# Performance work log

Measured on AMD Instinct MI355X. Metric: run time of the kernel, lower is better.

The kernel has to match this reference:

```python
import jax, jax.numpy as jnp
import numpy as np

B, N, DIM, HEADS = 8, 512, 512, 16
MAX_DIST, NG = 128, 32
RBF_STOP = 20.0
EPS = 1e-5


def _ln(x, g, b):
    m = jnp.mean(x, axis=-1, keepdims=True)
    v = jnp.mean((x - m) ** 2, axis=-1, keepdims=True)
    return (x - m) * jax.lax.rsqrt(v + EPS) * g + b


def setup_inputs() -> dict:
    key = jax.random.key(0)
    ks = jax.random.split(key, 12)
    d = DIM
    s = 0.02
    return {
        "x": jax.random.normal(ks[0], (B * N, d), jnp.float32),
        "dist_matrix": jax.random.randint(ks[1], (B, N, N), 0, MAX_DIST, jnp.int32),
        "dist_3d": jax.random.uniform(ks[2], (B, N, N), jnp.float32) * RBF_STOP,
        "norm1_g": jnp.ones((d,), jnp.float32),
        "norm1_b": jnp.zeros((d,), jnp.float32),
        "in_proj_w": jax.random.normal(ks[3], (3 * d, d), jnp.float32) * s,
        "in_proj_b": jnp.zeros((3 * d,), jnp.float32),
        "out_proj_w": jax.random.normal(ks[4], (d, d), jnp.float32) * s,
        "out_proj_b": jnp.zeros((d,), jnp.float32),
        "dist_emb": jax.random.normal(ks[5], (MAX_DIST, HEADS), jnp.float32) * s,
        "rbf_w": jax.random.normal(ks[6], (HEADS, NG), jnp.float32) * s,
        "rbf_b": jnp.zeros((HEADS,), jnp.float32),
        "norm2_g": jnp.ones((d,), jnp.float32),
        "norm2_b": jnp.zeros((d,), jnp.float32),
        "ffn_w1": jax.random.normal(ks[7], (4 * d, d), jnp.float32) * s,
        "ffn_b1": jnp.zeros((4 * d,), jnp.float32),
        "ffn_w2": jax.random.normal(ks[8], (d, 4 * d), jnp.float32) * s,
        "ffn_b2": jnp.zeros((d,), jnp.float32),
        "batch": jnp.repeat(jnp.arange(B, dtype=jnp.int32), N),
    }


def reference(x, dist_matrix, dist_3d, norm1_g, norm1_b, in_proj_w, in_proj_b,
              out_proj_w, out_proj_b, dist_emb, rbf_w, rbf_b, norm2_g, norm2_b,
              ffn_w1, ffn_b1, ffn_w2, ffn_b2, batch):
    b, n = dist_matrix.shape[0], dist_matrix.shape[1]
    d = x.shape[-1]
    dh = d // HEADS
    # equal-size graphs -> to_dense_batch is a reshape, mask all-true
    xd = x.reshape(b, n, d)

    # additive attention bias: shortest-path-distance embedding + RBF projection
    dc = jnp.clip(dist_matrix, 0, MAX_DIST - 1)
    bias_spd = dist_emb[dc]                                  # [b, n, n, H]
    offset = jnp.linspace(0.0, RBF_STOP, NG, dtype=jnp.float32)
    coeff = -0.5 / (RBF_STOP / (NG - 1)) ** 2
    rbf = jnp.exp(coeff * (dist_3d[..., None] - offset) ** 2)  # [b, n, n, NG]
    bias_3d = rbf @ rbf_w.T + rbf_b                          # [b, n, n, H]
    bias = jnp.transpose(bias_spd + bias_3d, (0, 3, 1, 2))   # [b, H, n, n]

    # multi-head attention (pre-norm residual, as in source)
    h = _ln(xd, norm1_g, norm1_b)
    qkv = h @ in_proj_w.T + in_proj_b
    q, k, v = jnp.split(qkv, 3, axis=-1)
    q = q.reshape(b, n, HEADS, dh).transpose(0, 2, 1, 3)
    k = k.reshape(b, n, HEADS, dh).transpose(0, 2, 1, 3)
    v = v.reshape(b, n, HEADS, dh).transpose(0, 2, 1, 3)
    scores = jnp.einsum('bhqd,bhkd->bhqk', q, k) / jnp.sqrt(jnp.float32(dh)) + bias
    attn = jax.nn.softmax(scores, axis=-1)
    ctx = jnp.einsum('bhqk,bhkd->bhqd', attn, v)
    ctx = ctx.transpose(0, 2, 1, 3).reshape(b, n, d)
    attn_out = ctx @ out_proj_w.T + out_proj_b
    h = h + attn_out

    # FFN (dropout inactive at eval)
    h2 = _ln(h, norm2_g, norm2_b)
    ff = jax.nn.gelu(h2 @ ffn_w1.T + ffn_b1, approximate=False) @ ffn_w2.T + ffn_b2
    h = h + ff
    return h.reshape(b * n, d)
```

## Files before the change

kernel.cpp:

```cpp
#include <hip/hip_runtime.h>
#include <hip/hip_bf16.h>
#include <math.h>

#define BB 8
#define NN 512
#define DD 512
#define NH 16
#define DH 32
#define TD 1536
#define NG 32
#define MAXD 128

typedef __attribute__((ext_vector_type(8))) short bf16x8;
typedef __attribute__((ext_vector_type(4))) float f32x4;

__device__ inline short f2bf(float x) {
    __hip_bfloat16 h = __float2bfloat16(x);
    return *reinterpret_cast<short*>(&h);
}
__device__ inline float bf2f(short x) {
    union { unsigned u; float f; } c;
    c.u = ((unsigned)(unsigned short)x) << 16;
    return c.f;
}

__device__ inline void gld_lds16(const void* g, void* l) {
    __builtin_amdgcn_global_load_lds(
        (const __attribute__((address_space(1))) unsigned int*)g,
        (__attribute__((address_space(3))) unsigned int*)l, 16, 0, 0);
}

__global__ __launch_bounds__(256) void cvt_weights(
    const float* __restrict__ s0, const float* __restrict__ s1,
    const float* __restrict__ s2, const float* __restrict__ s3,
    short* __restrict__ d0, short* __restrict__ d1,
    short* __restrict__ d2, short* __restrict__ d3,
    int n0, int n1, int n2, int n3) {
    const float* s; short* d; int n;
    switch (blockIdx.y) {
        case 0: s = s0; d = d0; n = n0; break;
        case 1: s = s1; d = d1; n = n1; break;
        case 2: s = s2; d = d2; n = n2; break;
        default: s = s3; d = d3; n = n3; break;
    }
    const int i = (blockIdx.x * 256 + threadIdx.x) * 4;
    if (i >= n) return;
    const float4 v = *(const float4*)(s + i);
    short4 o;
    o.x = f2bf(v.x); o.y = f2bf(v.y); o.z = f2bf(v.z); o.w = f2bf(v.w);
    *(short4*)(d + i) = o;
}

__global__ __launch_bounds__(256) void rbf_table(
    const float* __restrict__ rbfw, const float* __restrict__ rbfb,
    short* __restrict__ Tg) {
    const int idx = blockIdx.x * 256 + threadIdx.x;
    if (idx >= 130 * 16) return;
    const int i = idx >> 4, h = idx & 15;
    const float STEP  = 20.0f / 31.0f;
    const float COEFF = -0.5f / (STEP * STEP);
    const float x = fminf((float)i, 128.0f) * (20.0f / 128.0f);
    float acc = rbfb[h];
#pragma unroll
    for (int g = 0; g < NG; g++) {
        const float t = x - (float)g * STEP;
        acc += __expf(COEFF * t * t) * rbfw[h * NG + g];
    }
    Tg[idx] = f2bf(acc);
}

__global__ __launch_bounds__(256) void ln_kernel(const float* __restrict__ x,
                                                 const float* __restrict__ g,
                                                 const float* __restrict__ b,
                                                 short* __restrict__ out_bf,
                                                 float* __restrict__ out_f) {
    const int row = blockIdx.x;
    const int tid = threadIdx.x;
    const float* xr = x + (size_t)row * DD;
    float v0 = xr[tid], v1 = xr[tid + 256];
    __shared__ float s1[256], s2[256];
    s1[tid] = v0 + v1;
    s2[tid] = v0 * v0 + v1 * v1;
    __syncthreads();
    for (int off = 128; off > 0; off >>= 1) {
        if (tid < off) { s1[tid] += s1[tid + off]; s2[tid] += s2[tid + off]; }
        __syncthreads();
    }
    const float mean = s1[0] * (1.0f / DD);
    const float var  = s2[0] * (1.0f / DD) - mean * mean;
    const float rs   = rsqrtf(var + 1e-5f);
    const float o0 = (v0 - mean) * rs * g[tid] + b[tid];
    const float o1 = (v1 - mean) * rs * g[tid + 256] + b[tid + 256];
    out_bf[(size_t)row * DD + tid]       = f2bf(o0);
    out_bf[(size_t)row * DD + tid + 256] = f2bf(o1);
    if (out_f) {
        out_f[(size_t)row * DD + tid]       = o0;
        out_f[(size_t)row * DD + tid + 256] = o1;
    }
}

template <int TM, bool GELU, bool RES, int OUT>
__global__ __launch_bounds__(256) void gemm_bf16(
    const short* __restrict__ A, const short* __restrict__ Bw,
    const float* __restrict__ bias, const float* __restrict__ res,
    void* __restrict__ Cout, int M, int Nout, int K) {
    const int MI = TM / 32;
    const int bm = blockIdx.y * TM;
    const int bn = blockIdx.x * 128;
    const int tid  = threadIdx.x;
    const int wave = tid >> 6;
    const int lane = tid & 63;
    const int l16  = lane & 15;
    const int quad = lane >> 4;
    const int wr = (wave >> 1) * (TM / 2);
    const int wc = (wave & 1) * 64;

    __shared__ short As[TM * 32];
    __shared__ short Bs[128 * 32];

    f32x4 acc[MI][4];
#pragma unroll
    for (int i = 0; i < MI; i++)
#pragma unroll
        for (int j = 0; j < 4; j++) acc[i][j] = (f32x4){0.f, 0.f, 0.f, 0.f};

    for (int k0 = 0; k0 < K; k0 += 32) {
        const short* Ab = A + (size_t)bm * K + k0;
        const short* Bb = Bw + (size_t)bn * K + k0;
#pragma unroll
        for (int j = 0; j < TM / 64; j++) {
            const int idx = j * 256 + wave * 64 + lane;
            gld_lds16(Ab + (size_t)(idx >> 2) * K + (idx & 3) * 8,
                      (short*)As + (size_t)(j * 256 + wave * 64) * 8);
        }
#pragma unroll
        for (int j = 0; j < 2; j++) {
            const int idx = j * 256 + wave * 64 + lane;
            gld_lds16(Bb + (size_t)(idx >> 2) * K + (idx & 3) * 8,
                      (short*)Bs + (size_t)(j * 256 + wave * 64) * 8);
        }
        __syncthreads();
        bf16x8 af[MI], bfr[4];
#pragma unroll
        for (int i = 0; i < MI; i++)
            af[i] = *(const bf16x8*)&As[(wr + i * 16 + l16) * 32 + quad * 8];
#pragma unroll
        for (int j = 0; j < 4; j++)
            bfr[j] = *(const bf16x8*)&Bs[(wc + j * 16 + l16) * 32 + quad * 8];
#pragma unroll
        for (int i = 0; i < MI; i++)
#pragma unroll
            for (int j = 0; j < 4; j++)
                acc[i][j] = __builtin_amdgcn_mfma_f32_16x16x32_bf16(af[i], bfr[j], acc[i][j], 0, 0, 0);
        __syncthreads();
    }
#pragma unroll
    for (int i = 0; i < MI; i++) {
#pragma unroll
        for (int r = 0; r < 4; r++) {
            const int row = bm + wr + i * 16 + quad * 4 + r;
#pragma unroll
            for (int j = 0; j < 4; j++) {
                const int col = bn + wc + j * 16 + l16;
                float v = acc[i][j][r] + bias[col];
                if (GELU) v = 0.5f * v * (1.0f + erff(v * 0.70710678118654752f));
                if (RES)  v += res[(size_t)row * Nout + col];
                if (OUT == 1) ((short*)Cout)[(size_t)row * Nout + col] = f2bf(v);
                else          ((float*)Cout)[(size_t)row * Nout + col] = v;
            }
        }
    }
}

__global__ __launch_bounds__(512) void attn_mfma(
    const short* __restrict__ qkv,
    const int* __restrict__ dist,
    const float* __restrict__ dist3d,
    const float* __restrict__ demb,
    const short* __restrict__ Tg,
    float* __restrict__ O_part,
    float* __restrict__ l_part)
{
    const int blk  = blockIdx.x;
    const int b    = blk & 7;
    const int t3   = blk >> 3;
    const int part = t3 % 3;
    const int q0   = (t3 / 3) * 16;
    const int tid  = threadIdx.x;
    const int wave = tid >> 6;
    const int lane = tid & 63;
    const int l16  = lane & 15;
    const int quad = lane >> 4;

    __shared__ short Kc[NH * 16 * 32];
    __shared__ short Vc[NH * 16 * 32];
    __shared__ short Pb[8 * 16 * 32];
    __shared__ short Tt[130 * 18];
    __shared__ short Db[128 * 18];

    for (int i = tid; i < 8 * 16 * 32; i += 512) Pb[i] = 0;
    for (int i = tid; i < 130 * 16; i += 512) Tt[(i >> 4) * 18 + (i & 15)] = Tg[i];
    for (int i = tid; i < 128 * 16; i += 512) Db[(i >> 4) * 18 + (i & 15)] = f2bf(demb[i]);

    const float scale = 0.17677669529663687f;
    bf16x8 qf[2];
#pragma unroll
    for (int h = 0; h < 2; h++) {
        const int hh = wave * 2 + h;
        qf[h] = *(const bf16x8*)(qkv + (size_t)(b * NN + q0 + l16) * TD + hh * DH + quad * 8);
    }

    f32x4 O[2][2];
    float lsum[2][4];
#pragma unroll
    for (int h = 0; h < 2; h++) {
#pragma unroll
        for (int tt = 0; tt < 2; tt++) O[h][tt] = (f32x4){0.f, 0.f, 0.f, 0.f};
#pragma unroll
        for (int r = 0; r < 4; r++) lsum[h][r] = 0.f;
    }

    const int cbeg = part * 11;
    const int cend = (part == 2) ? 32 : cbeg + 11;

    for (int c = cbeg; c < cend; c++) {
        const int k0 = c * 16;
        __syncthreads();
#pragma unroll
        for (int l = 0; l < 4; l++) {
            const int idxb = l * 512 + wave * 64;
            const int idx  = idxb + lane;
            const int kk2  = idx & 1023;
            const int h = kk2 >> 6, k = (kk2 >> 2) & 15, c4 = kk2 & 3;
            const short* src = qkv + (size_t)(b * NN + k0 + k) * TD +
                               DD * (1 + (l >> 1)) + h * 32 + c4 * 8;
            short* dstb = (l < 2 ? (short*)Kc : (short*)Vc) + (size_t)(idxb & 1023) * 8;
            gld_lds16(src, dstb);
        }
        float biasr[2][4];
        {
            const int hh0 = wave * 2, hh1 = hh0 + 1;
#pragma unroll
            for (int r = 0; r < 4; r++) {
                const size_t off = ((size_t)(b * NN) + q0 + quad * 4 + r) * NN + k0 + l16;
                int dc = dist[off];
                dc = min(max(dc, 0), MAXD - 1);
                const float x = dist3d[off] * 6.4f;
                int ii = (int)x; ii = min(ii, 127);
                const float fr = x - (float)ii;
                const float t00 = bf2f(Tt[ii * 18 + hh0]), t01 = bf2f(Tt[ii * 18 + 18 + hh0]);
                const float t10 = bf2f(Tt[ii * 18 + hh1]), t11 = bf2f(Tt[ii * 18 + 18 + hh1]);
                biasr[0][r] = bf2f(Db[dc * 18 + hh0]) + t00 + (t01 - t00) * fr;
                biasr[1][r] = bf2f(Db[dc * 18 + hh1]) + t10 + (t11 - t10) * fr;
            }
        }
        __syncthreads();
#pragma unroll
        for (int h = 0; h < 2; h++) {
            const int hh = wave * 2 + h;
            const bf16x8 kf = *(const bf16x8*)&Kc[hh * 512 + l16 * 32 + quad * 8];
            f32x4 s = __builtin_amdgcn_mfma_f32_16x16x32_bf16(
                qf[h], kf, (f32x4){0.f, 0.f, 0.f, 0.f}, 0, 0, 0);
            float pv[4];
#pragma unroll
            for (int r = 0; r < 4; r++) {
                float sv = s[r] * scale + biasr[h][r];
                sv = fminf(sv, 20.f);
                pv[r] = __expf(sv);
                lsum[h][r] += pv[r];
                Pb[wave * 512 + (quad * 4 + r) * 32 + l16] = f2bf(pv[r]);
            }
            const bf16x8 pf = *(const bf16x8*)&Pb[wave * 512 + l16 * 32 + quad * 8];
#pragma unroll
            for (int tt = 0; tt < 2; tt++) {
                bf16x8 vf;
                if (quad < 2) {
#pragma unroll
                    for (int j = 0; j < 8; j++)
                        vf[j] = Vc[hh * 512 + (quad * 8 + j) * 32 + tt * 16 + l16];
                } else {
#pragma unroll
                    for (int j = 0; j < 8; j++) vf[j] = 0;
                }
                O[h][tt] = __builtin_amdgcn_mfma_f32_16x16x32_bf16(pf, vf, O[h][tt], 0, 0, 0);
            }
        }
    }
    const size_t poff = (size_t)part * 4096;
#pragma unroll
    for (int h = 0; h < 2; h++) {
        const int hh = wave * 2 + h;
#pragma unroll
        for (int m = 1; m < 16; m <<= 1)
#pragma unroll
            for (int r = 0; r < 4; r++) lsum[h][r] += __shfl_xor(lsum[h][r], m);
#pragma unroll
        for (int r = 0; r < 4; r++) {
            const size_t row = (size_t)(b * NN + q0 + quad * 4 + r);
#pragma unroll
            for (int tt = 0; tt < 2; tt++)
                O_part[(poff + row) * DD + hh * DH + tt * 16 + l16] = O[h][tt][r];
            if (l16 == 0) l_part[(poff + row) * NH + hh] = lsum[h][r];
        }
    }
}

__global__ __launch_bounds__(256) void attn_combine(
    const float* __restrict__ O_part, const float* __restrict__ l_part,
    short* __restrict__ ctx) {
    const int e = (blockIdx.x * 256 + threadIdx.x) * 4;
    const int row = e >> 9, d = e & 511, h = d >> 5;
    const size_t PO = (size_t)4096 * 512;
    const float4 o0 = *(const float4*)(O_part + e);
    const float4 o1 = *(const float4*)(O_part + PO + e);
    const float4 o2 = *(const float4*)(O_part + 2 * PO + e);
    const int li = row * NH + h;
    const float l = l_part[li] + l_part[4096 * NH + li] + l_part[2 * 4096 * NH + li];
    const float rinv = 1.0f / l;
    short4 o;
    o.x = f2bf((o0.x + o1.x + o2.x) * rinv);
    o.y = f2bf((o0.y + o1.y + o2.y) * rinv);
    o.z = f2bf((o0.z + o1.z + o2.z) * rinv);
    o.w = f2bf((o0.w + o1.w + o2.w) * rinv);
    *(short4*)(ctx + e) = o;
}

extern "C" void kernel_launch(void* const* d_in, const int* in_sizes, int n_in,
                              void* d_out, int out_size, void* d_ws, size_t ws_size,
                              hipStream_t stream) {
    const float* x      = (const float*)d_in[0];
    const int*   dist   = (const int*)d_in[1];
    const float* dist3d = (const float*)d_in[2];
    const float* n1g    = (const float*)d_in[3];
    const float* n1b    = (const float*)d_in[4];
    const float* win    = (const float*)d_in[5];
    const float* bin    = (const float*)d_in[6];
    const float* wo     = (const float*)d_in[7];
    const float* bo     = (const float*)d_in[8];
    const float* demb   = (const float*)d_in[9];
    const float* rbfw   = (const float*)d_in[10];
    const float* rbfb   = (const float*)d_in[11];
    const float* n2g    = (const float*)d_in[12];
    const float* n2b    = (const float*)d_in[13];
    const float* w1     = (const float*)d_in[14];
    const float* b1     = (const float*)d_in[15];
    const float* w2     = (const float*)d_in[16];
    const float* b2     = (const float*)d_in[17];

    char* p = (char*)d_ws;
    short* h_bf   = (short*)p; p += (size_t)4096 * 512 * 2;
    float* h_f    = (float*)p; p += (size_t)4096 * 512 * 4;
    short* qkv_bf = (short*)p; p += (size_t)4096 * 1536 * 2;
    short* ctx_bf = (short*)p; p += (size_t)4096 * 512 * 2;
    float* hres   = (float*)p; p += (size_t)4096 * 512 * 4;
    short* h2_bf  = (short*)p; p += (size_t)4096 * 512 * 2;
    short* win_bf = (short*)p; p += (size_t)1536 * 512 * 2;
    short* wo_bf  = (short*)p; p += (size_t)512 * 512 * 2;
    short* w1_bf  = (short*)p; p += (size_t)2048 * 512 * 2;
    short* w2_bf  = (short*)p; p += (size_t)512 * 2048 * 2;
    short* Tg     = (short*)p; p += (size_t)8192;
    float* O_part = (float*)p;
    short* mid_bf = (short*)p;
    p += (size_t)3 * 4096 * 512 * 4;
    float* l_part = (float*)p; p += (size_t)3 * 4096 * 16 * 4;

    const int M = BB * NN;

    cvt_weights<<<dim3(1024, 4), 256, 0, stream>>>(
        win, wo, w1, w2, win_bf, wo_bf, w1_bf, w2_bf,
        1536 * 512, 512 * 512, 2048 * 512, 512 * 2048);
    rbf_table<<<9, 256, 0, stream>>>(rbfw, rbfb, Tg);
    ln_kernel<<<M, 256, 0, stream>>>(x, n1g, n1b, h_bf, h_f);
    gemm_bf16<128, false, false, 1><<<dim3(12, 32), 256, 0, stream>>>(
        h_bf, win_bf, bin, nullptr, qkv_bf, M, TD, DD);
    attn_mfma<<<768, 512, 0, stream>>>(
        qkv_bf, dist, dist3d, demb, Tg, O_part, l_part);
    attn_combine<<<2048, 256, 0, stream>>>(O_part, l_part, ctx_bf);
    gemm_bf16<64, false, true, 0><<<dim3(4, 64), 256, 0, stream>>>(
        ctx_bf, wo_bf, bo, h_f, hres, M, DD, DD);
    ln_kernel<<<M, 256, 0, stream>>>(hres, n2g, n2b, h2_bf, nullptr);
    gemm_bf16<128, true, false, 1><<<dim3(16, 32), 256, 0, stream>>>(
        h2_bf, w1_bf, b1, nullptr, mid_bf, M, 2048, DD);
    gemm_bf16<64, false, true, 0><<<dim3(4, 64), 256, 0, stream>>>(
        mid_bf, w2_bf, b2, hres, (float*)d_out, M, DD, 2048);
}
```

Measured before the change: 267.2 us.

## Double-buffer GEMM LDS, shuffle-reduce layernorm, pad P buffer, fuse RBF table launch

The GEMM now double-buffers its LDS tiles, so the next K slice is fetched while the current one is multiplied, and it needs one barrier per iteration instead of two. LayerNorm swaps its shared-memory tree reduction for wavefront shuffle reductions. The attention P scratch buffer gets a padded row stride to reduce LDS bank conflicts, and the RBF table build moves into the weight-conversion kernel to save one launch. The QKV and FFN1 GEMMs switch to 64-row tiles for more blocks, at the cost of less reuse per block and more LDS per block from double buffering.

New measurement: 262.2 us. No clear change (-1.9%).

```diff
diff --git a/kernel.cpp b/kernel.cpp
--- a/kernel.cpp
+++ b/kernel.cpp
@@ -35,7 +35,26 @@
     const float* __restrict__ s2, const float* __restrict__ s3,
     short* __restrict__ d0, short* __restrict__ d1,
     short* __restrict__ d2, short* __restrict__ d3,
+    const float* __restrict__ rbfw, const float* __restrict__ rbfb,
+    short* __restrict__ Tg,
     int n0, int n1, int n2, int n3) {
+    if (blockIdx.y == 4) {
+        if (blockIdx.x != 0) return;
+        const float STEP  = 20.0f / 31.0f;
+        const float COEFF = -0.5f / (STEP * STEP);
+        for (int idx = threadIdx.x; idx < 130 * 16; idx += 256) {
+            const int i = idx >> 4, h = idx & 15;
+            const float x = fminf((float)i, 128.0f) * (20.0f / 128.0f);
+            float acc = rbfb[h];
+#pragma unroll
+            for (int g = 0; g < NG; g++) {
+                const float t = x - (float)g * STEP;
+                acc += __expf(COEFF * t * t) * rbfw[h * NG + g];
+            }
+            Tg[idx] = f2bf(acc);
+        }
+        return;
+    }
     const float* s; short* d; int n;
     switch (blockIdx.y) {
         case 0: s = s0; d = d0; n = n0; break;
@@ -49,24 +68,6 @@
     short4 o;
     o.x = f2bf(v.x); o.y = f2bf(v.y); o.z = f2bf(v.z); o.w = f2bf(v.w);
     *(short4*)(d + i) = o;
-}
-
-__global__ __launch_bounds__(256) void rbf_table(
-    const float* __restrict__ rbfw, const float* __restrict__ rbfb,
-    short* __restrict__ Tg) {
-    const int idx = blockIdx.x * 256 + threadIdx.x;
-    if (idx >= 130 * 16) return;
-    const int i = idx >> 4, h = idx & 15;
-    const float STEP  = 20.0f / 31.0f;
-    const float COEFF = -0.5f / (STEP * STEP);
-    const float x = fminf((float)i, 128.0f) * (20.0f / 128.0f);
-    float acc = rbfb[h];
-#pragma unroll
-    for (int g = 0; g < NG; g++) {
-        const float t = x - (float)g * STEP;
-        acc += __expf(COEFF * t * t) * rbfw[h * NG + g];
-    }
-    Tg[idx] = f2bf(acc);
 }
 
 __global__ __launch_bounds__(256) void ln_kernel(const float* __restrict__ x,
@@ -76,18 +77,19 @@
                                                  float* __restrict__ out_f) {
     const int row = blockIdx.x;
     const int tid = threadIdx.x;
+    const int wave = tid >> 6, lane = tid & 63;
     const float* xr = x + (size_t)row * DD;
-    float v0 = xr[tid], v1 = xr[tid + 256];
-    __shared__ float s1[256], s2[256];
-    s1[tid] = v0 + v1;
-    s2[tid] = v0 * v0 + v1 * v1;
+    const float v0 = xr[tid], v1 = xr[tid + 256];
+    float s = v0 + v1, q = v0 * v0 + v1 * v1;
+#pragma unroll
+    for (int m = 1; m < 64; m <<= 1) { s += __shfl_xor(s, m); q += __shfl_xor(q, m); }
+    __shared__ float ps[8];
+    if (lane == 0) { ps[wave] = s; ps[wave + 4] = q; }
     __syncthreads();
-    for (int off = 128; off > 0; off >>= 1) {
-        if (tid < off) { s1[tid] += s1[tid + off]; s2[tid] += s2[tid + off]; }
-        __syncthreads();
-    }
-    const float mean = s1[0] * (1.0f / DD);
-    const float var  = s2[0] * (1.0f / DD) - mean * mean;
+    s = ps[0] + ps[1] + ps[2] + ps[3];
+    q = ps[4] + ps[5] + ps[6] + ps[7];
+    const float mean = s * (1.0f / DD);
+    const float var  = q * (1.0f / DD) - mean * mean;
     const float rs   = rsqrtf(var + 1e-5f);
     const float o0 = (v0 - mean) * rs * g[tid] + b[tid];
     const float o1 = (v1 - mean) * rs * g[tid + 256] + b[tid + 256];
@@ -115,8 +117,8 @@
     const int wr = (wave >> 1) * (TM / 2);
     const int wc = (wave & 1) * 64;
 
-    __shared__ short As[TM * 32];
-    __shared__ short Bs[128 * 32];
+    __shared__ short As[2][TM * 32];
+    __shared__ short Bs[2][128 * 32];
 
     f32x4 acc[MI][4];
 #pragma unroll
@@ -124,36 +126,48 @@
 #pragma unroll
         for (int j = 0; j < 4; j++) acc[i][j] = (f32x4){0.f, 0.f, 0.f, 0.f};
 
-    for (int k0 = 0; k0 < K; k0 += 32) {
+    auto stage = [&](int buf, int k0) {
         const short* Ab = A + (size_t)bm * K + k0;
         const short* Bb = Bw + (size_t)bn * K + k0;
 #pragma unroll
         for (int j = 0; j < TM / 64; j++) {
             const int idx = j * 256 + wave * 64 + lane;
             gld_lds16(Ab + (size_t)(idx >> 2) * K + (idx & 3) * 8,
-                      (short*)As + (size_t)(j * 256 + wave * 64) * 8);
+                      &As[buf][(size_t)(j * 256 + wave * 64) * 8]);
         }
 #pragma unroll
         for (int j = 0; j < 2; j++) {
             const int idx = j * 256 + wave * 64 + lane;
             gld_lds16(Bb + (size_t)(idx >> 2) * K + (idx & 3) * 8,
-                      (short*)Bs + (size_t)(j * 256 + wave * 64) * 8);
-        }
-        __syncthreads();
+                      &Bs[buf][(size_t)(j * 256 + wave * 64) * 8]);
+        }
+    };
+    auto compute = [&](int buf) {
         bf16x8 af[MI], bfr[4];
 #pragma unroll
         for (int i = 0; i < MI; i++)
-            af[i] = *(const bf16x8*)&As[(wr + i * 16 + l16) * 32 + quad * 8];
+            af[i] = *(const bf16x8*)&As[buf][(wr + i * 16 + l16) * 32 + quad * 8];
 #pragma unroll
         for (int j = 0; j < 4; j++)
-            bfr[j] = *(const bf16x8*)&Bs[(wc + j * 16 + l16) * 32 + quad * 8];
+            bfr[j] = *(const bf16x8*)&Bs[buf][(wc + j * 16 + l16) * 32 + quad * 8];
 #pragma unroll
         for (int i = 0; i < MI; i++)
 #pragma unroll
             for (int j = 0; j < 4; j++)
                 acc[i][j] = __builtin_amdgcn_mfma_f32_16x16x32_bf16(af[i], bfr[j], acc[i][j], 0, 0, 0);
+    };
+
+    stage(0, 0);
+    __syncthreads();
+    int cur = 0;
+    for (int k0 = 32; k0 < K; k0 += 32) {
+        stage(cur ^ 1, k0);
+        compute(cur);
         __syncthreads();
-    }
+        cur ^= 1;
+    }
+    compute(cur);
+
 #pragma unroll
     for (int i = 0; i < MI; i++) {
 #pragma unroll
@@ -194,11 +208,11 @@
 
     __shared__ short Kc[NH * 16 * 32];
     __shared__ short Vc[NH * 16 * 32];
-    __shared__ short Pb[8 * 16 * 32];
+    __shared__ short Pb[8 * 16 * 34];
     __shared__ short Tt[130 * 18];
     __shared__ short Db[128 * 18];
 
-    for (int i = tid; i < 8 * 16 * 32; i += 512) Pb[i] = 0;
+    for (int i = tid; i < 8 * 16 * 34; i += 512) Pb[i] = 0;
     for (int i = tid; i < 130 * 16; i += 512) Tt[(i >> 4) * 18 + (i & 15)] = Tg[i];
     for (int i = tid; i < 128 * 16; i += 512) Db[(i >> 4) * 18 + (i & 15)] = f2bf(demb[i]);
 
@@ -268,9 +282,9 @@
                 sv = fminf(sv, 20.f);
                 pv[r] = __expf(sv);
                 lsum[h][r] += pv[r];
-                Pb[wave * 512 + (quad * 4 + r) * 32 + l16] = f2bf(pv[r]);
-            }
-            const bf16x8 pf = *(const bf16x8*)&Pb[wave * 512 + l16 * 32 + quad * 8];
+                Pb[wave * 544 + (quad * 4 + r) * 34 + l16] = f2bf(pv[r]);
+            }
+            const bf16x8 pf = *(const bf16x8*)&Pb[wave * 544 + l16 * 34 + quad * 8];
 #pragma unroll
             for (int tt = 0; tt < 2; tt++) {
                 bf16x8 vf;
@@ -366,12 +380,11 @@
 
     const int M = BB * NN;
 
-    cvt_weights<<<dim3(1024, 4), 256, 0, stream>>>(
-        win, wo, w1, w2, win_bf, wo_bf, w1_bf, w2_bf,
+    cvt_weights<<<dim3(1024, 5), 256, 0, stream>>>(
+        win, wo, w1, w2, win_bf, wo_bf, w1_bf, w2_bf, rbfw, rbfb, Tg,
         1536 * 512, 512 * 512, 2048 * 512, 512 * 2048);
-    rbf_table<<<9, 256, 0, stream>>>(rbfw, rbfb, Tg);
     ln_kernel<<<M, 256, 0, stream>>>(x, n1g, n1b, h_bf, h_f);
-    gemm_bf16<128, false, false, 1><<<dim3(12, 32), 256, 0, stream>>>(
+    gemm_bf16<64, false, false, 1><<<dim3(12, 64), 256, 0, stream>>>(
         h_bf, win_bf, bin, nullptr, qkv_bf, M, TD, DD);
     attn_mfma<<<768, 512, 0, stream>>>(
         qkv_bf, dist, dist3d, demb, Tg, O_part, l_part);
@@ -379,7 +392,7 @@
     gemm_bf16<64, false, true, 0><<<dim3(4, 64), 256, 0, stream>>>(
         ctx_bf, wo_bf, bo, h_f, hres, M, DD, DD);
     ln_kernel<<<M, 256, 0, stream>>>(hres, n2g, n2b, h2_bf, nullptr);
-    gemm_bf16<128, true, false, 1><<<dim3(16, 32), 256, 0, stream>>>(
+    gemm_bf16<64, true, false, 1><<<dim3(16, 64), 256, 0, stream>>>(
         h2_bf, w1_bf, b1, nullptr, mid_bf, M, 2048, DD);
     gemm_bf16<64, false, true, 0><<<dim3(4, 64), 256, 0, stream>>>(
         mid_bf, w2_bf, b2, hres, (float*)d_out, M, DD, 2048);
```
